# Optimization experiments

Hardware: AMD Instinct MI355X
Metric: run time of the kernel (lower is better)

## Reference

```python
import jax, jax.numpy as jnp
import numpy as np

B, X, Y, Z = 8, 32, 32, 32
Dx = Dy = Dz = 128
K = 256   # h_dim * k, k=1
H = 2     # h_out
EPS = 1e-5


def _wn(V, g):
    # weight_norm with dim=None: W = g * V / ||V||_F (g scalar)
    return (g / jnp.linalg.norm(V)) * V


def setup_inputs() -> dict:
    key = jax.random.key(0)
    ks = jax.random.split(key, 8)
    x = jax.random.normal(ks[0], (B, X, Dx), jnp.float32)
    y = jax.random.normal(ks[1], (B, Y, Dy), jnp.float32)
    z = jax.random.normal(ks[2], (B, Z, Dz), jnp.float32)
    Vx = jax.random.normal(ks[3], (K, Dx), jnp.float32) * 0.05
    Vy = jax.random.normal(ks[4], (K, Dy), jnp.float32) * 0.05
    Vz = jax.random.normal(ks[5], (K, Dz), jnp.float32) * 0.05
    Vh = jax.random.normal(ks[6], (H, K), jnp.float32) * 0.05
    return {
        "x": x, "y": y, "z": z,
        "Vx": Vx, "gx": jnp.linalg.norm(Vx), "bx": jnp.zeros((K,), jnp.float32),
        "Vy": Vy, "gy": jnp.linalg.norm(Vy), "by": jnp.zeros((K,), jnp.float32),
        "Vz": Vz, "gz": jnp.linalg.norm(Vz), "bz": jnp.zeros((K,), jnp.float32),
        "Vh": Vh, "gh": jnp.linalg.norm(Vh), "bh": jnp.zeros((H,), jnp.float32),
        "gamma": jnp.ones((K,), jnp.float32), "beta": jnp.zeros((K,), jnp.float32),
    }


def reference(x, y, z, Vx, gx, bx, Vy, gy, by, Vz, gz, bz, Vh, gh, bh, gamma, beta):
    relu = jax.nn.relu
    _x = relu(x @ _wn(Vx, gx).T + bx)  # [B,X,K]
    _y = relu(y @ _wn(Vy, gy).T + by)  # [B,Y,K]
    _z = relu(z @ _wn(Vz, gz).T + bz)  # [B,Z,K]
    # trilinear outer product: [B,X,Y,Z,K] (memory-explosive intermediate)
    xyz = jnp.einsum('bxk,byk,bzk->bxyzk', _x, _y, _z)
    att = jnp.einsum('bxyzk,hk->bhxyz', xyz, _wn(Vh, gh)) + bh[None, :, None, None, None]
    # softmax over flattened X*Y*Z per head
    att = jax.nn.softmax(att.reshape(B, H, -1), axis=-1).reshape(B, H, X, Y, Z)
    # attention pooling, summed over all h_out heads (equals the torch loop)
    att_sum = att.sum(axis=1)  # [B,X,Y,Z]
    logits = jnp.einsum('bxk,byk,bzk,bxyz->bk', _x, _y, _z, att_sum)  # [B,K]
    # BatchNorm1d (training-mode batch stats, biased variance)
    mean = logits.mean(axis=0)
    var = logits.var(axis=0)
    out = (logits - mean) / jnp.sqrt(var + EPS) * gamma + beta
    return (out, att)
```

## Files before the change

kernel.cpp:

```cpp
#include <hip/hip_runtime.h>
#include <math.h>

#define BB 8
#define DD 128
#define KK 256
#define XYZ 32768
#define EPSV 1e-5f

#define WS_X     0
#define WS_Y     65536
#define WS_Z     131072
#define WS_RAW   196608
#define WS_SM    (WS_RAW + 524288)
#define WS_PART  (WS_SM + 1024)

__global__ void __launch_bounds__(256)
tan_proj_kernel(const float* x, const float* y, const float* z,
                const float* Vx, const float* Vy, const float* Vz,
                const float* gx, const float* gy, const float* gz,
                const float* bx, const float* by, const float* bz,
                float* ws) {
    __shared__ float lin[4 * DD];
    __shared__ float wred[4];
    int bid = blockIdx.x;
    int t = threadIdx.x;
    int which = bid >> 6;
    int rgrp = bid & 63;
    int r0 = rgrp * 4;
    const float *in, *V, *g, *bias;
    float* outp;
    if (which == 0)      { in = x; V = Vx; g = gx; bias = bx; outp = ws + WS_X; }
    else if (which == 1) { in = y; V = Vy; g = gy; bias = by; outp = ws + WS_Y; }
    else                 { in = z; V = Vz; g = gz; bias = bz; outp = ws + WS_Z; }
    {
        int f0 = t, f1 = t + 256;
        lin[f0] = in[(r0 + (f0 >> 7)) * DD + (f0 & 127)];
        lin[f1] = in[(r0 + (f1 >> 7)) * DD + (f1 & 127)];
    }
    __syncthreads();
    const float4* v4 = (const float4*)(V + t * DD);
    const float4* l4 = (const float4*)lin;
    float a0 = 0.f, a1 = 0.f, a2 = 0.f, a3 = 0.f, ssp = 0.f;
#pragma unroll 8
    for (int d4 = 0; d4 < DD / 4; ++d4) {
        float4 a = v4[d4];
        ssp += a.x * a.x + a.y * a.y + a.z * a.z + a.w * a.w;
        float4 b0 = l4[d4];
        float4 b1 = l4[32 + d4];
        float4 b2 = l4[64 + d4];
        float4 b3 = l4[96 + d4];
        a0 += a.x * b0.x + a.y * b0.y + a.z * b0.z + a.w * b0.w;
        a1 += a.x * b1.x + a.y * b1.y + a.z * b1.z + a.w * b1.w;
        a2 += a.x * b2.x + a.y * b2.y + a.z * b2.z + a.w * b2.w;
        a3 += a.x * b3.x + a.y * b3.y + a.z * b3.z + a.w * b3.w;
    }
#pragma unroll
    for (int o = 32; o > 0; o >>= 1) ssp += __shfl_xor(ssp, o);
    if ((t & 63) == 0) wred[t >> 6] = ssp;
    __syncthreads();
    float ss = wred[0] + wred[1] + wred[2] + wred[3];
    float scale = g[0] * rsqrtf(ss);
    float bv = bias[t];
    outp[(r0 + 0) * KK + t] = fmaxf(a0 * scale + bv, 0.f);
    outp[(r0 + 1) * KK + t] = fmaxf(a1 * scale + bv, 0.f);
    outp[(r0 + 2) * KK + t] = fmaxf(a2 * scale + bv, 0.f);
    outp[(r0 + 3) * KK + t] = fmaxf(a3 * scale + bv, 0.f);
}

__global__ void __launch_bounds__(256)
tan_score_kernel(const float* Vh, const float* gh, const float* bh, float* ws) {
    __shared__ float ys[32 * 256];
    __shared__ float zs[32 * 256];
    __shared__ float shh;
    __shared__ float smred[4][4];
    int t = threadIdx.x;
    int bb = blockIdx.x >> 5;
    int xx = blockIdx.x & 31;
    const float* _xb = ws + WS_X + (bb * 32 + xx) * KK;
    const float* _yb = ws + WS_Y + bb * 8192;
    const float* _zb = ws + WS_Z + bb * 8192;

    if (t < 64) {
        float4 h1 = *(const float4*)(Vh + t * 8);
        float4 h2 = *(const float4*)(Vh + t * 8 + 4);
        float hs = h1.x * h1.x + h1.y * h1.y + h1.z * h1.z + h1.w * h1.w
                 + h2.x * h2.x + h2.y * h2.y + h2.z * h2.z + h2.w * h2.w;
#pragma unroll
        for (int o = 32; o > 0; o >>= 1) hs += __shfl_xor(hs, o);
        if (t == 0) shh = hs;
    }

#pragma unroll
    for (int i = 0; i < 8; ++i) {
        int flat = i * 1024 + t * 4;
        int row = flat >> 8;
        int k = flat & 255;
        int gsw = (((k >> 2) ^ (row & 7)) << 2);
        *(float4*)(ys + row * 256 + gsw) = *(const float4*)(_yb + flat);
        *(float4*)(zs + row * 256 + gsw) = *(const float4*)(_zb + flat);
    }
    __syncthreads();
    float sh = gh[0] * rsqrtf(shh);

    int ty = t >> 4;
    int tz = t & 15;
    int y0 = ty, y1 = ty + 16;
    int z0 = tz, z1 = tz + 16;
    int ysw0 = (y0 & 7), ysw1 = (y1 & 7);
    int zsw0 = (z0 & 7), zsw1 = (z1 & 7);

    float a000 = 0.f, a001 = 0.f, a010 = 0.f, a011 = 0.f;
    float a100 = 0.f, a101 = 0.f, a110 = 0.f, a111 = 0.f;

#pragma unroll 4
    for (int kc = 0; kc < 256; kc += 4) {
        int g = kc >> 2;
        float4 xv  = *(const float4*)(_xb + kc);
        float4 vh0 = *(const float4*)(Vh + kc);
        float4 vh1 = *(const float4*)(Vh + KK + kc);
        float4 ya = *(const float4*)(ys + y0 * 256 + ((g ^ ysw0) << 2));
        float4 yb = *(const float4*)(ys + y1 * 256 + ((g ^ ysw1) << 2));
        float4 za = *(const float4*)(zs + z0 * 256 + ((g ^ zsw0) << 2));
        float4 zb = *(const float4*)(zs + z1 * 256 + ((g ^ zsw1) << 2));
#define TAN_STEP(c) { \
        float xs = sh * xv.c; \
        float w0 = xs * vh0.c, w1 = xs * vh1.c; \
        float t00 = w0 * ya.c, t01 = w0 * yb.c; \
        float t10 = w1 * ya.c, t11 = w1 * yb.c; \
        a000 = fmaf(t00, za.c, a000); a001 = fmaf(t00, zb.c, a001); \
        a010 = fmaf(t01, za.c, a010); a011 = fmaf(t01, zb.c, a011); \
        a100 = fmaf(t10, za.c, a100); a101 = fmaf(t10, zb.c, a101); \
        a110 = fmaf(t11, za.c, a110); a111 = fmaf(t11, zb.c, a111); }
        TAN_STEP(x) TAN_STEP(y) TAN_STEP(z) TAN_STEP(w)
#undef TAN_STEP
    }

    float b0 = bh[0], b1 = bh[1];
    a000 += b0; a001 += b0; a010 += b0; a011 += b0;
    a100 += b1; a101 += b1; a110 += b1; a111 += b1;
    float* r0 = ws + WS_RAW + (bb * 2 + 0) * XYZ + xx * 1024;
    float* r1 = r0 + XYZ;
    r0[y0 * 32 + z0] = a000;  r0[y0 * 32 + z1] = a001;
    r0[y1 * 32 + z0] = a010;  r0[y1 * 32 + z1] = a011;
    r1[y0 * 32 + z0] = a100;  r1[y0 * 32 + z1] = a101;
    r1[y1 * 32 + z0] = a110;  r1[y1 * 32 + z1] = a111;

    float m0 = fmaxf(fmaxf(a000, a001), fmaxf(a010, a011));
    float l0 = __expf(a000 - m0) + __expf(a001 - m0)
             + __expf(a010 - m0) + __expf(a011 - m0);
    float m1 = fmaxf(fmaxf(a100, a101), fmaxf(a110, a111));
    float l1 = __expf(a100 - m1) + __expf(a101 - m1)
             + __expf(a110 - m1) + __expf(a111 - m1);
#pragma unroll
    for (int o = 1; o < 64; o <<= 1) {
        float mo = __shfl_xor(m0, o), lo = __shfl_xor(l0, o);
        float nm = fmaxf(m0, mo);
        l0 = l0 * __expf(m0 - nm) + lo * __expf(mo - nm); m0 = nm;
        mo = __shfl_xor(m1, o); lo = __shfl_xor(l1, o);
        nm = fmaxf(m1, mo);
        l1 = l1 * __expf(m1 - nm) + lo * __expf(mo - nm); m1 = nm;
    }
    if ((t & 63) == 0) {
        int w = t >> 6;
        smred[w][0] = m0; smred[w][1] = l0;
        smred[w][2] = m1; smred[w][3] = l1;
    }
    __syncthreads();
    if (t == 0) {
        float M0 = smred[0][0], L0 = smred[0][1];
        float M1 = smred[0][2], L1 = smred[0][3];
#pragma unroll
        for (int w = 1; w < 4; ++w) {
            float nm = fmaxf(M0, smred[w][0]);
            L0 = L0 * __expf(M0 - nm) + smred[w][1] * __expf(smred[w][0] - nm);
            M0 = nm;
            nm = fmaxf(M1, smred[w][2]);
            L1 = L1 * __expf(M1 - nm) + smred[w][3] * __expf(smred[w][2] - nm);
            M1 = nm;
        }
        float* sm = ws + WS_SM + (bb * 32 + xx) * 4;
        sm[0] = M0; sm[1] = L0; sm[2] = M1; sm[3] = L1;
    }
}

__global__ void __launch_bounds__(256)
tan_logits_kernel(float* ws, float* out) {
    __shared__ float as4[1024];
    __shared__ float cons[4];
    int b = blockIdx.x >> 5;
    int x = blockIdx.x & 31;
    int t = threadIdx.x;
    const float* _zb = ws + WS_Z + b * 8192;
    float zreg[32];
#pragma unroll
    for (int zi = 0; zi < 32; ++zi) zreg[zi] = _zb[zi * 256 + t];

    if (t < 64) {
        const float* sm = ws + WS_SM + (b * 32 + (t & 31)) * 4;
        float4 p = *(const float4*)sm;
        float m0 = p.x, l0 = p.y, m1 = p.z, l1 = p.w;
#pragma unroll
        for (int o = 1; o < 32; o <<= 1) {
            float mo = __shfl_xor(m0, o), lo = __shfl_xor(l0, o);
            float nm = fmaxf(m0, mo);
            l0 = l0 * __expf(m0 - nm) + lo * __expf(mo - nm); m0 = nm;
            mo = __shfl_xor(m1, o); lo = __shfl_xor(l1, o);
            nm = fmaxf(m1, mo);
            l1 = l1 * __expf(m1 - nm) + lo * __expf(mo - nm); m1 = nm;
        }
        if (t == 0) {
            cons[0] = m0; cons[1] = 1.f / l0;
            cons[2] = m1; cons[3] = 1.f / l1;
        }
    }
    __syncthreads();
    float M0 = cons[0], inv0 = cons[1], M1 = cons[2], inv1 = cons[3];
    const float* r0 = ws + WS_RAW + (b * 2) * XYZ + x * 1024;
    const float* r1 = r0 + XYZ;
    float* o0 = out + BB * KK + (b * 2) * XYZ + x * 1024;
    float* o1 = o0 + XYZ;
#pragma unroll
    for (int i = t; i < 1024; i += 256) {
        float a0 = __expf(r0[i] - M0) * inv0;
        float a1 = __expf(r1[i] - M1) * inv1;
        o0[i] = a0; o1[i] = a1;
        as4[i] = a0 + a1;
    }
    __syncthreads();

    const float* _yb = ws + WS_Y + b * 8192;
    float acc = 0.f;
#pragma unroll 4
    for (int y = 0; y < 32; ++y) {
        float s = 0.f;
        const float4* ar = (const float4*)(as4 + y * 32);
#pragma unroll
        for (int j = 0; j < 8; ++j) {
            float4 a = ar[j];
            s += a.x * zreg[j * 4] + a.y * zreg[j * 4 + 1]
               + a.z * zreg[j * 4 + 2] + a.w * zreg[j * 4 + 3];
        }
        acc = fmaf(_yb[y * 256 + t], s, acc);
    }
    float xv = ws[WS_X + (b * 32 + x) * 256 + t];
    ws[WS_PART + (b * 32 + x) * 256 + t] = xv * acc;
}

__global__ void __launch_bounds__(1024)
tan_bn_kernel(const float* ws, const float* gamma, const float* beta, float* out) {
    __shared__ float red[8192];
    int t = threadIdx.x;
    int tg = t >> 8;
    int k = t & 255;
    const float* part = ws + WS_PART;
    float lg[BB];
#pragma unroll
    for (int b = 0; b < BB; ++b) {
        float s = 0.f;
#pragma unroll
        for (int xi = 0; xi < 8; ++xi)
            s += part[(b * 32 + tg * 8 + xi) * 256 + k];
        red[tg * 2048 + b * 256 + k] = s;
    }
    __syncthreads();
    if (tg == 0) {
#pragma unroll
        for (int b = 0; b < BB; ++b)
            lg[b] = red[b * 256 + k] + red[2048 + b * 256 + k]
                  + red[4096 + b * 256 + k] + red[6144 + b * 256 + k];
        float mean = 0.f;
#pragma unroll
        for (int b = 0; b < BB; ++b) mean += lg[b];
        mean *= 0.125f;
        float var = 0.f;
#pragma unroll
        for (int b = 0; b < BB; ++b) { float d = lg[b] - mean; var += d * d; }
        var *= 0.125f;
        float inv = rsqrtf(var + EPSV);
        float gm = gamma[k], bt = beta[k];
#pragma unroll
        for (int b = 0; b < BB; ++b)
            out[b * 256 + k] = (lg[b] - mean) * inv * gm + bt;
    }
}

extern "C" void kernel_launch(void* const* d_in, const int* in_sizes, int n_in,
                              void* d_out, int out_size, void* d_ws, size_t ws_size,
                              hipStream_t stream) {
    (void)in_sizes; (void)n_in; (void)out_size; (void)ws_size;
    const float* x     = (const float*)d_in[0];
    const float* y     = (const float*)d_in[1];
    const float* z     = (const float*)d_in[2];
    const float* Vx    = (const float*)d_in[3];
    const float* gx    = (const float*)d_in[4];
    const float* bx    = (const float*)d_in[5];
    const float* Vy    = (const float*)d_in[6];
    const float* gy    = (const float*)d_in[7];
    const float* by    = (const float*)d_in[8];
    const float* Vz    = (const float*)d_in[9];
    const float* gz    = (const float*)d_in[10];
    const float* bz    = (const float*)d_in[11];
    const float* Vh    = (const float*)d_in[12];
    const float* gh    = (const float*)d_in[13];
    const float* bh    = (const float*)d_in[14];
    const float* gamma = (const float*)d_in[15];
    const float* beta  = (const float*)d_in[16];
    float* ws  = (float*)d_ws;
    float* out = (float*)d_out;

    tan_proj_kernel<<<192, 256, 0, stream>>>(x, y, z, Vx, Vy, Vz,
                                             gx, gy, gz, bx, by, bz, ws);
    tan_score_kernel<<<256, 256, 0, stream>>>(Vh, gh, bh, ws);
    tan_logits_kernel<<<256, 256, 0, stream>>>(ws, out);
    tan_bn_kernel<<<1, 1024, 0, stream>>>(ws, gamma, beta, out);
}
```

Measured before the change: 121.7 us.

## Fuse all four stages into one cooperative kernel with grid syncs

Merges projection, score, softmax-normalize/pooling and batchnorm into a single cooperative launch separated by grid-wide syncs. Raw attention scores now stay in registers across the grid sync instead of a round trip through a workspace buffer, and y/z rows are reused from shared memory already loaded for scoring. This removes three kernel launches and the raw-score write and read, at the cost of grid-sync overhead and higher shared-memory use per block. The final batchnorm runs on a single block reducing 32 partials per batch.

Result: slower. 226.9 us (+86.5%).

```diff
diff --git a/kernel.cpp b/kernel.cpp
--- a/kernel.cpp
+++ b/kernel.cpp
@@ -1,5 +1,8 @@
 #include <hip/hip_runtime.h>
+#include <hip/hip_cooperative_groups.h>
 #include <math.h>
+
+namespace cg = cooperative_groups;
 
 #define BB 8
 #define DD 128
@@ -10,72 +13,81 @@
 #define WS_X     0
 #define WS_Y     65536
 #define WS_Z     131072
-#define WS_RAW   196608
-#define WS_SM    (WS_RAW + 524288)
-#define WS_PART  (WS_SM + 1024)
+#define WS_SM    196608
+#define WS_PART  197632
 
 __global__ void __launch_bounds__(256)
-tan_proj_kernel(const float* x, const float* y, const float* z,
-                const float* Vx, const float* Vy, const float* Vz,
-                const float* gx, const float* gy, const float* gz,
-                const float* bx, const float* by, const float* bz,
-                float* ws) {
+tan_fused_kernel(const float* __restrict__ x, const float* __restrict__ y,
+                 const float* __restrict__ z,
+                 const float* __restrict__ Vx, const float* __restrict__ Vy,
+                 const float* __restrict__ Vz,
+                 const float* __restrict__ gx, const float* __restrict__ gy,
+                 const float* __restrict__ gz,
+                 const float* __restrict__ bx, const float* __restrict__ by,
+                 const float* __restrict__ bz,
+                 const float* __restrict__ Vh, const float* __restrict__ gh,
+                 const float* __restrict__ bh,
+                 const float* __restrict__ gamma, const float* __restrict__ beta,
+                 float* __restrict__ ws, float* __restrict__ out) {
+    cg::grid_group grid = cg::this_grid();
+    __shared__ float ys[32 * 256];
+    __shared__ float zs[32 * 256];
+    __shared__ float as4[1024];
     __shared__ float lin[4 * DD];
     __shared__ float wred[4];
+    __shared__ float smred[4][4];
+    __shared__ float cons[4];
+    __shared__ float shh;
     int bid = blockIdx.x;
     int t = threadIdx.x;
-    int which = bid >> 6;
-    int rgrp = bid & 63;
-    int r0 = rgrp * 4;
-    const float *in, *V, *g, *bias;
-    float* outp;
-    if (which == 0)      { in = x; V = Vx; g = gx; bias = bx; outp = ws + WS_X; }
-    else if (which == 1) { in = y; V = Vy; g = gy; bias = by; outp = ws + WS_Y; }
-    else                 { in = z; V = Vz; g = gz; bias = bz; outp = ws + WS_Z; }
-    {
-        int f0 = t, f1 = t + 256;
-        lin[f0] = in[(r0 + (f0 >> 7)) * DD + (f0 & 127)];
-        lin[f1] = in[(r0 + (f1 >> 7)) * DD + (f1 & 127)];
-    }
-    __syncthreads();
-    const float4* v4 = (const float4*)(V + t * DD);
-    const float4* l4 = (const float4*)lin;
-    float a0 = 0.f, a1 = 0.f, a2 = 0.f, a3 = 0.f, ssp = 0.f;
+
+    if (bid < 192) {
+        int which = bid >> 6;
+        int rgrp = bid & 63;
+        int r0 = rgrp * 4;
+        const float *in, *V, *g, *bias;
+        float* outp;
+        if (which == 0)      { in = x; V = Vx; g = gx; bias = bx; outp = ws + WS_X; }
+        else if (which == 1) { in = y; V = Vy; g = gy; bias = by; outp = ws + WS_Y; }
+        else                 { in = z; V = Vz; g = gz; bias = bz; outp = ws + WS_Z; }
+        {
+            int f0 = t, f1 = t + 256;
+            lin[f0] = in[(r0 + (f0 >> 7)) * DD + (f0 & 127)];
+            lin[f1] = in[(r0 + (f1 >> 7)) * DD + (f1 & 127)];
+        }
+        __syncthreads();
+        const float4* v4 = (const float4*)(V + t * DD);
+        const float4* l4 = (const float4*)lin;
+        float a0 = 0.f, a1 = 0.f, a2 = 0.f, a3 = 0.f, ssp = 0.f;
 #pragma unroll 8
-    for (int d4 = 0; d4 < DD / 4; ++d4) {
-        float4 a = v4[d4];
-        ssp += a.x * a.x + a.y * a.y + a.z * a.z + a.w * a.w;
-        float4 b0 = l4[d4];
-        float4 b1 = l4[32 + d4];
-        float4 b2 = l4[64 + d4];
-        float4 b3 = l4[96 + d4];
-        a0 += a.x * b0.x + a.y * b0.y + a.z * b0.z + a.w * b0.w;
-        a1 += a.x * b1.x + a.y * b1.y + a.z * b1.z + a.w * b1.w;
-        a2 += a.x * b2.x + a.y * b2.y + a.z * b2.z + a.w * b2.w;
-        a3 += a.x * b3.x + a.y * b3.y + a.z * b3.z + a.w * b3.w;
-    }
-#pragma unroll
-    for (int o = 32; o > 0; o >>= 1) ssp += __shfl_xor(ssp, o);
-    if ((t & 63) == 0) wred[t >> 6] = ssp;
-    __syncthreads();
-    float ss = wred[0] + wred[1] + wred[2] + wred[3];
-    float scale = g[0] * rsqrtf(ss);
-    float bv = bias[t];
-    outp[(r0 + 0) * KK + t] = fmaxf(a0 * scale + bv, 0.f);
-    outp[(r0 + 1) * KK + t] = fmaxf(a1 * scale + bv, 0.f);
-    outp[(r0 + 2) * KK + t] = fmaxf(a2 * scale + bv, 0.f);
-    outp[(r0 + 3) * KK + t] = fmaxf(a3 * scale + bv, 0.f);
-}
-
-__global__ void __launch_bounds__(256)
-tan_score_kernel(const float* Vh, const float* gh, const float* bh, float* ws) {
-    __shared__ float ys[32 * 256];
-    __shared__ float zs[32 * 256];
-    __shared__ float shh;
-    __shared__ float smred[4][4];
-    int t = threadIdx.x;
-    int bb = blockIdx.x >> 5;
-    int xx = blockIdx.x & 31;
+        for (int d4 = 0; d4 < DD / 4; ++d4) {
+            float4 a = v4[d4];
+            ssp += a.x * a.x + a.y * a.y + a.z * a.z + a.w * a.w;
+            float4 b0 = l4[d4];
+            float4 b1 = l4[32 + d4];
+            float4 b2 = l4[64 + d4];
+            float4 b3 = l4[96 + d4];
+            a0 += a.x * b0.x + a.y * b0.y + a.z * b0.z + a.w * b0.w;
+            a1 += a.x * b1.x + a.y * b1.y + a.z * b1.z + a.w * b1.w;
+            a2 += a.x * b2.x + a.y * b2.y + a.z * b2.z + a.w * b2.w;
+            a3 += a.x * b3.x + a.y * b3.y + a.z * b3.z + a.w * b3.w;
+        }
+#pragma unroll
+        for (int o = 32; o > 0; o >>= 1) ssp += __shfl_xor(ssp, o);
+        if ((t & 63) == 0) wred[t >> 6] = ssp;
+        __syncthreads();
+        float ss = wred[0] + wred[1] + wred[2] + wred[3];
+        float scale = g[0] * rsqrtf(ss);
+        float bv = bias[t];
+        outp[(r0 + 0) * KK + t] = fmaxf(a0 * scale + bv, 0.f);
+        outp[(r0 + 1) * KK + t] = fmaxf(a1 * scale + bv, 0.f);
+        outp[(r0 + 2) * KK + t] = fmaxf(a2 * scale + bv, 0.f);
+        outp[(r0 + 3) * KK + t] = fmaxf(a3 * scale + bv, 0.f);
+    }
+    grid.sync();
+
+    int bb = bid >> 5;
+    int xx = bid & 31;
     const float* _xb = ws + WS_X + (bb * 32 + xx) * KK;
     const float* _yb = ws + WS_Y + bb * 8192;
     const float* _zb = ws + WS_Z + bb * 8192;
@@ -138,65 +150,49 @@
     float b0 = bh[0], b1 = bh[1];
     a000 += b0; a001 += b0; a010 += b0; a011 += b0;
     a100 += b1; a101 += b1; a110 += b1; a111 += b1;
-    float* r0 = ws + WS_RAW + (bb * 2 + 0) * XYZ + xx * 1024;
-    float* r1 = r0 + XYZ;
-    r0[y0 * 32 + z0] = a000;  r0[y0 * 32 + z1] = a001;
-    r0[y1 * 32 + z0] = a010;  r0[y1 * 32 + z1] = a011;
-    r1[y0 * 32 + z0] = a100;  r1[y0 * 32 + z1] = a101;
-    r1[y1 * 32 + z0] = a110;  r1[y1 * 32 + z1] = a111;
-
-    float m0 = fmaxf(fmaxf(a000, a001), fmaxf(a010, a011));
-    float l0 = __expf(a000 - m0) + __expf(a001 - m0)
-             + __expf(a010 - m0) + __expf(a011 - m0);
-    float m1 = fmaxf(fmaxf(a100, a101), fmaxf(a110, a111));
-    float l1 = __expf(a100 - m1) + __expf(a101 - m1)
-             + __expf(a110 - m1) + __expf(a111 - m1);
-#pragma unroll
-    for (int o = 1; o < 64; o <<= 1) {
-        float mo = __shfl_xor(m0, o), lo = __shfl_xor(l0, o);
-        float nm = fmaxf(m0, mo);
-        l0 = l0 * __expf(m0 - nm) + lo * __expf(mo - nm); m0 = nm;
-        mo = __shfl_xor(m1, o); lo = __shfl_xor(l1, o);
-        nm = fmaxf(m1, mo);
-        l1 = l1 * __expf(m1 - nm) + lo * __expf(mo - nm); m1 = nm;
-    }
-    if ((t & 63) == 0) {
-        int w = t >> 6;
-        smred[w][0] = m0; smred[w][1] = l0;
-        smred[w][2] = m1; smred[w][3] = l1;
-    }
-    __syncthreads();
-    if (t == 0) {
-        float M0 = smred[0][0], L0 = smred[0][1];
-        float M1 = smred[0][2], L1 = smred[0][3];
-#pragma unroll
-        for (int w = 1; w < 4; ++w) {
-            float nm = fmaxf(M0, smred[w][0]);
-            L0 = L0 * __expf(M0 - nm) + smred[w][1] * __expf(smred[w][0] - nm);
-            M0 = nm;
-            nm = fmaxf(M1, smred[w][2]);
-            L1 = L1 * __expf(M1 - nm) + smred[w][3] * __expf(smred[w][2] - nm);
-            M1 = nm;
-        }
-        float* sm = ws + WS_SM + (bb * 32 + xx) * 4;
-        sm[0] = M0; sm[1] = L0; sm[2] = M1; sm[3] = L1;
-    }
-}
-
-__global__ void __launch_bounds__(256)
-tan_logits_kernel(float* ws, float* out) {
-    __shared__ float as4[1024];
-    __shared__ float cons[4];
-    int b = blockIdx.x >> 5;
-    int x = blockIdx.x & 31;
-    int t = threadIdx.x;
-    const float* _zb = ws + WS_Z + b * 8192;
-    float zreg[32];
-#pragma unroll
-    for (int zi = 0; zi < 32; ++zi) zreg[zi] = _zb[zi * 256 + t];
+
+    {
+        float m0 = fmaxf(fmaxf(a000, a001), fmaxf(a010, a011));
+        float l0 = __expf(a000 - m0) + __expf(a001 - m0)
+                 + __expf(a010 - m0) + __expf(a011 - m0);
+        float m1 = fmaxf(fmaxf(a100, a101), fmaxf(a110, a111));
+        float l1 = __expf(a100 - m1) + __expf(a101 - m1)
+                 + __expf(a110 - m1) + __expf(a111 - m1);
+#pragma unroll
+        for (int o = 1; o < 64; o <<= 1) {
+            float mo = __shfl_xor(m0, o), lo = __shfl_xor(l0, o);
+            float nm = fmaxf(m0, mo);
+            l0 = l0 * __expf(m0 - nm) + lo * __expf(mo - nm); m0 = nm;
+            mo = __shfl_xor(m1, o); lo = __shfl_xor(l1, o);
+            nm = fmaxf(m1, mo);
+            l1 = l1 * __expf(m1 - nm) + lo * __expf(mo - nm); m1 = nm;
+        }
+        if ((t & 63) == 0) {
+            int w = t >> 6;
+            smred[w][0] = m0; smred[w][1] = l0;
+            smred[w][2] = m1; smred[w][3] = l1;
+        }
+        __syncthreads();
+        if (t == 0) {
+            float M0 = smred[0][0], L0 = smred[0][1];
+            float M1 = smred[0][2], L1 = smred[0][3];
+#pragma unroll
+            for (int w = 1; w < 4; ++w) {
+                float nm = fmaxf(M0, smred[w][0]);
+                L0 = L0 * __expf(M0 - nm) + smred[w][1] * __expf(smred[w][0] - nm);
+                M0 = nm;
+                nm = fmaxf(M1, smred[w][2]);
+                L1 = L1 * __expf(M1 - nm) + smred[w][3] * __expf(smred[w][2] - nm);
+                M1 = nm;
+            }
+            float* sm = ws + WS_SM + (bb * 32 + xx) * 4;
+            sm[0] = M0; sm[1] = L0; sm[2] = M1; sm[3] = L1;
+        }
+    }
+    grid.sync();
 
     if (t < 64) {
-        const float* sm = ws + WS_SM + (b * 32 + (t & 31)) * 4;
+        const float* sm = ws + WS_SM + (bb * 32 + (t & 31)) * 4;
         float4 p = *(const float4*)sm;
         float m0 = p.x, l0 = p.y, m1 = p.z, l1 = p.w;
 #pragma unroll
@@ -215,59 +211,61 @@
     }
     __syncthreads();
     float M0 = cons[0], inv0 = cons[1], M1 = cons[2], inv1 = cons[3];
-    const float* r0 = ws + WS_RAW + (b * 2) * XYZ + x * 1024;
-    const float* r1 = r0 + XYZ;
-    float* o0 = out + BB * KK + (b * 2) * XYZ + x * 1024;
+
+    float e000 = __expf(a000 - M0) * inv0, e001 = __expf(a001 - M0) * inv0;
+    float e010 = __expf(a010 - M0) * inv0, e011 = __expf(a011 - M0) * inv0;
+    float e100 = __expf(a100 - M1) * inv1, e101 = __expf(a101 - M1) * inv1;
+    float e110 = __expf(a110 - M1) * inv1, e111 = __expf(a111 - M1) * inv1;
+
+    float* o0 = out + BB * KK + (bb * 2 + 0) * XYZ + xx * 1024;
     float* o1 = o0 + XYZ;
-#pragma unroll
-    for (int i = t; i < 1024; i += 256) {
-        float a0 = __expf(r0[i] - M0) * inv0;
-        float a1 = __expf(r1[i] - M1) * inv1;
-        o0[i] = a0; o1[i] = a1;
-        as4[i] = a0 + a1;
-    }
+    o0[y0 * 32 + z0] = e000;  o0[y0 * 32 + z1] = e001;
+    o0[y1 * 32 + z0] = e010;  o0[y1 * 32 + z1] = e011;
+    o1[y0 * 32 + z0] = e100;  o1[y0 * 32 + z1] = e101;
+    o1[y1 * 32 + z0] = e110;  o1[y1 * 32 + z1] = e111;
+
+    as4[y0 * 32 + z0] = e000 + e100;  as4[y0 * 32 + z1] = e001 + e101;
+    as4[y1 * 32 + z0] = e010 + e110;  as4[y1 * 32 + z1] = e011 + e111;
     __syncthreads();
 
-    const float* _yb = ws + WS_Y + b * 8192;
-    float acc = 0.f;
+    {
+        float zreg[32], yreg[32];
+        int gi = t >> 2, ci = t & 3;
+#pragma unroll
+        for (int r = 0; r < 32; ++r) {
+            int sw = (((gi ^ (r & 7)) << 2) | ci);
+            zreg[r] = zs[r * 256 + sw];
+            yreg[r] = ys[r * 256 + sw];
+        }
+        float acc = 0.f;
 #pragma unroll 4
-    for (int y = 0; y < 32; ++y) {
-        float s = 0.f;
-        const float4* ar = (const float4*)(as4 + y * 32);
-#pragma unroll
-        for (int j = 0; j < 8; ++j) {
-            float4 a = ar[j];
-            s += a.x * zreg[j * 4] + a.y * zreg[j * 4 + 1]
-               + a.z * zreg[j * 4 + 2] + a.w * zreg[j * 4 + 3];
-        }
-        acc = fmaf(_yb[y * 256 + t], s, acc);
-    }
-    float xv = ws[WS_X + (b * 32 + x) * 256 + t];
-    ws[WS_PART + (b * 32 + x) * 256 + t] = xv * acc;
-}
-
-__global__ void __launch_bounds__(1024)
-tan_bn_kernel(const float* ws, const float* gamma, const float* beta, float* out) {
-    __shared__ float red[8192];
-    int t = threadIdx.x;
-    int tg = t >> 8;
-    int k = t & 255;
-    const float* part = ws + WS_PART;
-    float lg[BB];
-#pragma unroll
-    for (int b = 0; b < BB; ++b) {
-        float s = 0.f;
-#pragma unroll
-        for (int xi = 0; xi < 8; ++xi)
-            s += part[(b * 32 + tg * 8 + xi) * 256 + k];
-        red[tg * 2048 + b * 256 + k] = s;
-    }
-    __syncthreads();
-    if (tg == 0) {
-#pragma unroll
-        for (int b = 0; b < BB; ++b)
-            lg[b] = red[b * 256 + k] + red[2048 + b * 256 + k]
-                  + red[4096 + b * 256 + k] + red[6144 + b * 256 + k];
+        for (int yy = 0; yy < 32; ++yy) {
+            float s = 0.f;
+            const float4* ar = (const float4*)(as4 + yy * 32);
+#pragma unroll
+            for (int j = 0; j < 8; ++j) {
+                float4 a = ar[j];
+                s += a.x * zreg[j * 4] + a.y * zreg[j * 4 + 1]
+                   + a.z * zreg[j * 4 + 2] + a.w * zreg[j * 4 + 3];
+            }
+            acc = fmaf(yreg[yy], s, acc);
+        }
+        float xv = _xb[t];
+        ws[WS_PART + (bb * 32 + xx) * 256 + t] = xv * acc;
+    }
+    grid.sync();
+
+    if (bid == 0) {
+        const float* part = ws + WS_PART;
+        float lg[BB];
+#pragma unroll
+        for (int b = 0; b < BB; ++b) {
+            float s = 0.f;
+#pragma unroll
+            for (int xi = 0; xi < 32; ++xi)
+                s += part[(b * 32 + xi) * 256 + t];
+            lg[b] = s;
+        }
         float mean = 0.f;
 #pragma unroll
         for (int b = 0; b < BB; ++b) mean += lg[b];
@@ -277,10 +275,10 @@
         for (int b = 0; b < BB; ++b) { float d = lg[b] - mean; var += d * d; }
         var *= 0.125f;
         float inv = rsqrtf(var + EPSV);
-        float gm = gamma[k], bt = beta[k];
+        float gm = gamma[t], bt = beta[t];
 #pragma unroll
         for (int b = 0; b < BB; ++b)
-            out[b * 256 + k] = (lg[b] - mean) * inv * gm + bt;
+            out[b * 256 + t] = (lg[b] - mean) * inv * gm + bt;
     }
 }
 
@@ -308,9 +306,15 @@
     float* ws  = (float*)d_ws;
     float* out = (float*)d_out;
 
-    tan_proj_kernel<<<192, 256, 0, stream>>>(x, y, z, Vx, Vy, Vz,
-                                             gx, gy, gz, bx, by, bz, ws);
-    tan_score_kernel<<<256, 256, 0, stream>>>(Vh, gh, bh, ws);
-    tan_logits_kernel<<<256, 256, 0, stream>>>(ws, out);
-    tan_bn_kernel<<<1, 1024, 0, stream>>>(ws, gamma, beta, out);
+    void* args[] = {
+        (void*)&x, (void*)&y, (void*)&z,
+        (void*)&Vx, (void*)&Vy, (void*)&Vz,
+        (void*)&gx, (void*)&gy, (void*)&gz,
+        (void*)&bx, (void*)&by, (void*)&bz,
+        (void*)&Vh, (void*)&gh, (void*)&bh,
+        (void*)&gamma, (void*)&beta,
+        (void*)&ws, (void*)&out
+    };
+    hipLaunchCooperativeKernel((const void*)tan_fused_kernel,
+                               dim3(256), dim3(256), args, 0, stream);
 }
```
